# Kernel optimization log

Hardware: AMD Instinct MI355X
Metric: run time of the kernel (lower is better)

Reference implementation:

```python
import jax, jax.numpy as jnp
import numpy as np

B, S, D, H = 2, 2048, 1024, 16
DK = D // H


def setup_inputs() -> dict:
    key = jax.random.key(0)
    ks = jax.random.split(key, 11)
    scale = 1.0 / np.sqrt(D)
    inp = {
        'q': jax.random.normal(ks[0], (B, S, D), jnp.float32),
        'k': jax.random.normal(ks[1], (B, S, D), jnp.float32),
        'v': jax.random.normal(ks[2], (B, S, D), jnp.float32),
        'mask': jnp.tril(jnp.ones((S, S), jnp.int32))[None, None],  # [1,1,S,S] causal
        'w_q': jax.random.normal(ks[3], (D, D), jnp.float32) * scale,
        'b_q': jax.random.normal(ks[4], (D,), jnp.float32) * scale,
        'w_k': jax.random.normal(ks[5], (D, D), jnp.float32) * scale,
        'b_k': jax.random.normal(ks[6], (D,), jnp.float32) * scale,
        'w_v': jax.random.normal(ks[7], (D, D), jnp.float32) * scale,
        'b_v': jax.random.normal(ks[8], (D,), jnp.float32) * scale,
        'w_o': jax.random.normal(ks[9], (D, D), jnp.float32) * scale,
        'b_o': jax.random.normal(ks[10], (D,), jnp.float32) * scale,
    }
    return inp


def reference(q, k, v, mask, w_q, b_q, w_k, b_k, w_v, b_v, w_o, b_o):
    # Linear projections (torch Linear: x @ W^T + b; here weights stored as [D_in, D_out])
    query = q @ w_q + b_q  # [B,S,D]
    key_ = k @ w_k + b_k
    value = v @ w_v + b_v
    # split heads -> [B,H,S,DK]
    def split(x):
        return x.reshape(B, S, H, DK).transpose(0, 2, 1, 3)
    qh, kh, vh = split(query), split(key_), split(value)
    scores = jnp.einsum('bhqd,bhkd->bhqk', qh, kh) / jnp.sqrt(jnp.float32(DK))
    scores = jnp.where(mask == 0, jnp.float32(-1e9), scores)
    attn = jax.nn.softmax(scores, axis=-1)  # dropout p=0.0 -> identity
    out = jnp.einsum('bhqk,bhkd->bhqd', attn, vh)  # [B,H,S,DK]
    out = out.transpose(0, 2, 1, 3).reshape(B, S, D)
    return out @ w_o + b_o
```

## Files before the change

### kernel.cpp

```cpp
#include <hip/hip_runtime.h>

typedef unsigned short u16;
typedef unsigned int u32;
typedef __attribute__((ext_vector_type(8))) short short8;
typedef __attribute__((ext_vector_type(4))) float f32x4;
typedef __attribute__((ext_vector_type(16))) float f32x16;
typedef __attribute__((ext_vector_type(4))) float float4v;
typedef __attribute__((ext_vector_type(4))) u16 u16x4;
typedef __attribute__((ext_vector_type(2))) u32 u32x2;

#define DEV static __device__ __forceinline__

static constexpr int S_LEN = 2048;
static constexpr int D_MODEL = 1024;
static constexpr int N_HEADS = 16;
static constexpr int DK = 64;
static constexpr float LOG2E = 1.4426950408889634f;
static constexpr float SM_SHIFT = 12.0f;

#if defined(__has_builtin)
#if __has_builtin(__builtin_amdgcn_exp2f)
#define EXP2(x) __builtin_amdgcn_exp2f(x)
#else
#define EXP2(x) exp2f(x)
#endif
#else
#define EXP2(x) exp2f(x)
#endif

DEV u16 f2bf(float f) {
  u32 u = __builtin_bit_cast(u32, f);
  u32 r = (u + 0x7FFFu + ((u >> 16) & 1u)) >> 16;
  return (u16)r;
}

DEV u32 pk2bf(float lo, float hi) {
  u32 d;
  asm("v_cvt_pk_bf16_f32 %0, %1, %2" : "=v"(d) : "v"(lo), "v"(hi));
  return d;
}

DEV void swap32(u32& a, u32& b) {
  asm volatile("v_permlane32_swap_b32 %0, %1" : "+v"(a), "+v"(b));
}

DEV short8 mk8(u32 w0, u32 w1, u32 w2, u32 w3) {
  union { u32 u[4]; short8 s; } t;
  t.u[0] = w0; t.u[1] = w1; t.u[2] = w2; t.u[3] = w3;
  return t.s;
}

DEV void async16(const void* g, void* l) {
  __builtin_amdgcn_global_load_lds(
      (const __attribute__((address_space(1))) u32*)g,
      (__attribute__((address_space(3))) u32*)l, 16, 0, 0);
}

DEV short8 lds_frag(const u16* tile, int row, int byteInRow) {
  const char* p = (const char*)tile + row * 128 + (byteInRow ^ ((row & 7) << 4));
  return *(const short8*)p;
}

DEV f32x4 mfma16(short8 a, short8 b, f32x4 c) {
  return __builtin_amdgcn_mfma_f32_16x16x32_bf16(a, b, c, 0, 0, 0);
}

DEV f32x16 mfma32(short8 a, short8 b, f32x16 c) {
  return __builtin_amdgcn_mfma_f32_32x32x16_bf16(a, b, c, 0, 0, 0);
}

__global__ void k_cvt3(const float* __restrict__ q, const float* __restrict__ k,
                       const float* __restrict__ v, u16* __restrict__ xq,
                       u16* __restrict__ xk, u16* __restrict__ xv, int n) {
  const float* src = blockIdx.y == 0 ? q : (blockIdx.y == 1 ? k : v);
  u16* dst = blockIdx.y == 0 ? xq : (blockIdx.y == 1 ? xk : xv);
  int i = (blockIdx.x * blockDim.x + threadIdx.x) * 4;
  int stride = gridDim.x * blockDim.x * 4;
  for (; i < n; i += stride) {
    float4v f = *(const float4v*)(src + i);
    u16x4 o;
    o[0] = f2bf(f[0]); o[1] = f2bf(f[1]); o[2] = f2bf(f[2]); o[3] = f2bf(f[3]);
    *(u16x4*)(dst + i) = o;
  }
}

__global__ void k_twz4(const float* __restrict__ wq, const float* __restrict__ wk,
                       const float* __restrict__ wv, const float* __restrict__ wo,
                       u16* __restrict__ tq, u16* __restrict__ tk,
                       u16* __restrict__ tv, u16* __restrict__ to_) {
  __shared__ u16 t[64][65];
  const int z = blockIdx.z;
  const float* W = z == 0 ? wq : (z == 1 ? wk : (z == 2 ? wv : wo));
  u16* Wt = z == 0 ? tq : (z == 1 ? tk : (z == 2 ? tv : to_));
  const int n0 = blockIdx.x * 64;
  const int k0 = blockIdx.y * 64;
  const int tid = threadIdx.x;
  const int c = tid & 63, r0 = tid >> 6;
#pragma unroll
  for (int j = 0; j < 16; ++j) {
    int r = r0 + j * 4;
    t[r][c] = f2bf(W[(size_t)(k0 + r) * D_MODEL + n0 + c]);
  }
  __syncthreads();
#pragma unroll
  for (int j = 0; j < 16; ++j) {
    int r = r0 + j * 4;
    Wt[(size_t)(n0 + r) * D_MODEL + k0 + c] = t[c][r];
  }
}

__global__ __launch_bounds__(256, 2) void k_gemm3(
    const u16* __restrict__ Xq, const u16* __restrict__ Xk, const u16* __restrict__ Xv,
    const u16* __restrict__ Wtq, const u16* __restrict__ Wtk, const u16* __restrict__ Wtv,
    const float* __restrict__ bq, const float* __restrict__ bk, const float* __restrict__ bv,
    u16* __restrict__ Qh, u16* __restrict__ Kh, u16* __restrict__ Vtp) {
  const int z = blockIdx.z;
  const u16* A = z == 0 ? Xq : (z == 1 ? Xk : Xv);
  const u16* Bt = z == 0 ? Wtq : (z == 1 ? Wtk : Wtv);
  const float* bias = z == 0 ? bq : (z == 1 ? bk : bv);
  u16* obf = z == 0 ? Qh : (z == 1 ? Kh : Vtp);
  const float scale = z == 0 ? 0.125f * LOG2E : 1.0f;

  __shared__ __align__(16) u16 As[128 * 64];
  __shared__ __align__(16) u16 Bs[128 * 64];
  const int tid = threadIdx.x;
  const int lane = tid & 63, w = tid >> 6;
  const int l15 = lane & 15, l4 = lane >> 4;
  const int bm = blockIdx.x * 128, bn = blockIdx.y * 128;
  const int wr = (w >> 1) * 64, wc = (w & 1) * 64;
  const int sr = tid >> 3, sc8 = tid & 7;
  f32x4 acc[4][4] = {};

  for (int k0 = 0; k0 < 1024; k0 += 64) {
    __syncthreads();
#pragma unroll
    for (int j = 0; j < 4; ++j) {
      int row = sr + j * 32;
      int col = (sc8 ^ (row & 7)) << 3;
      async16(A + (size_t)(bm + row) * 1024 + k0 + col, (char*)As + tid * 16 + j * 4096);
      async16(Bt + (size_t)(bn + row) * 1024 + k0 + col, (char*)Bs + tid * 16 + j * 4096);
    }
    __syncthreads();
    short8 af[4][2], bfv[4][2];
#pragma unroll
    for (int mi = 0; mi < 4; ++mi)
#pragma unroll
      for (int kk = 0; kk < 2; ++kk)
        af[mi][kk] = lds_frag(As, wr + mi * 16 + l15, kk * 64 + l4 * 16);
#pragma unroll
    for (int ni = 0; ni < 4; ++ni)
#pragma unroll
      for (int kk = 0; kk < 2; ++kk)
        bfv[ni][kk] = lds_frag(Bs, wc + ni * 16 + l15, kk * 64 + l4 * 16);
#pragma unroll
    for (int kk = 0; kk < 2; ++kk)
#pragma unroll
      for (int mi = 0; mi < 4; ++mi)
#pragma unroll
        for (int ni = 0; ni < 4; ++ni)
          acc[mi][ni] = mfma16(af[mi][kk], bfv[ni][kk], acc[mi][ni]);
  }

#pragma unroll
  for (int mi = 0; mi < 4; ++mi)
#pragma unroll
    for (int ni = 0; ni < 4; ++ni) {
      const int row0 = bm + wr + mi * 16 + l4 * 4;
      const int col = bn + wc + ni * 16 + l15;
      const int h = col >> 6, dk = col & 63;
      const int b = row0 >> 11, s0 = row0 & 2047;
      if (z == 2) {
        u16x4 pk;
#pragma unroll
        for (int r = 0; r < 4; ++r) pk[r] = f2bf(acc[mi][ni][r] + bias[col]);
        *(u16x4*)(obf + ((size_t)((b * N_HEADS + h) * DK + dk)) * S_LEN + s0) = pk;
      } else {
#pragma unroll
        for (int r = 0; r < 4; ++r) {
          float vv = (acc[mi][ni][r] + bias[col]) * scale;
          obf[(((size_t)(b * N_HEADS + h) * S_LEN + s0 + r) << 6) + dk] = f2bf(vv);
        }
      }
    }
}

__global__ __launch_bounds__(256, 2) void k_gemmO(
    const u16* __restrict__ A, const u16* __restrict__ Bt,
    const float* __restrict__ bias, float* __restrict__ ofp) {
  __shared__ __align__(16) u16 As[128 * 64];
  __shared__ __align__(16) u16 Bs[64 * 64];
  const int tid = threadIdx.x;
  const int lane = tid & 63, w = tid >> 6;
  const int l15 = lane & 15, l4 = lane >> 4;
  const int bm = blockIdx.x * 128, bn = blockIdx.y * 64;
  const int wr = w * 32;
  const int sr = tid >> 3, sc8 = tid & 7;
  f32x4 acc[2][4] = {};

  for (int k0 = 0; k0 < 1024; k0 += 64) {
    __syncthreads();
#pragma unroll
    for (int j = 0; j < 4; ++j) {
      int row = sr + j * 32;
      int col = (sc8 ^ (row & 7)) << 3;
      async16(A + (size_t)(bm + row) * 1024 + k0 + col, (char*)As + tid * 16 + j * 4096);
      if (j < 2)
        async16(Bt + (size_t)(bn + row) * 1024 + k0 + col, (char*)Bs + tid * 16 + j * 4096);
    }
    __syncthreads();
    short8 af[2][2], bfv[4][2];
#pragma unroll
    for (int mi = 0; mi < 2; ++mi)
#pragma unroll
      for (int kk = 0; kk < 2; ++kk)
        af[mi][kk] = lds_frag(As, wr + mi * 16 + l15, kk * 64 + l4 * 16);
#pragma unroll
    for (int ni = 0; ni < 4; ++ni)
#pragma unroll
      for (int kk = 0; kk < 2; ++kk)
        bfv[ni][kk] = lds_frag(Bs, ni * 16 + l15, kk * 64 + l4 * 16);
#pragma unroll
    for (int kk = 0; kk < 2; ++kk)
#pragma unroll
      for (int mi = 0; mi < 2; ++mi)
#pragma unroll
        for (int ni = 0; ni < 4; ++ni)
          acc[mi][ni] = mfma16(af[mi][kk], bfv[ni][kk], acc[mi][ni]);
  }

#pragma unroll
  for (int mi = 0; mi < 2; ++mi)
#pragma unroll
    for (int ni = 0; ni < 4; ++ni)
#pragma unroll
      for (int r = 0; r < 4; ++r) {
        int row = bm + wr + mi * 16 + l4 * 4 + r;
        int col = bn + ni * 16 + l15;
        ofp[(size_t)row * D_MODEL + col] = acc[mi][ni][r] + bias[col];
      }
}

__global__ __launch_bounds__(256, 3) void k_attn(
    const u16* __restrict__ Qh, const u16* __restrict__ Kh,
    const u16* __restrict__ Vt, u16* __restrict__ Om,
    float* __restrict__ Po, float* __restrict__ Pl) {
  __shared__ __align__(16) u16 Ks[2][64 * 64];
  __shared__ __align__(16) u16 Vs[2][64 * 64];
  const int tid = threadIdx.x;
  const int lane = tid & 63, w = tid >> 6;
  const int l31 = lane & 31, hf = lane >> 5;
  const int bid = blockIdx.x;

  int bh, g, c, tbeg, tend;
  bool partial;
  if (bid < 256) {
    bh = bid & 31; g = 8 + (bid >> 5); c = 0; tbeg = 0; tend = 16; partial = true;
  } else if (bid < 512) {
    int i = bid - 256;
    bh = i & 31; g = 15 - (i >> 5); c = 1; tbeg = 16; tend = 2 * g + 2; partial = true;
  } else {
    int i = bid - 512;
    bh = i & 31; g = 7 - (i >> 5); c = 0; tbeg = 0; tend = 2 * g + 2; partial = false;
  }

  const u16* Qb = Qh + (size_t)bh * S_LEN * DK;
  const u16* Kb = Kh + (size_t)bh * S_LEN * DK;
  const u16* Vb = Vt + (size_t)bh * DK * S_LEN;
  const int q0 = g * 128;
  const int qw = q0 + w * 32;
  const int sc8 = tid & 7;

  auto stage = [&](int t0, int buf) {
#pragma unroll
    for (int j = 0; j < 2; ++j) {
      int row = (tid >> 3) + j * 32;
      int col = (sc8 ^ (row & 7)) << 3;
      async16(Kb + (size_t)(t0 + row) * DK + col, (char*)Ks[buf] + tid * 16 + j * 4096);
      async16(Vb + (size_t)row * S_LEN + t0 + col, (char*)Vs[buf] + tid * 16 + j * 4096);
    }
  };

  short8 qB[4];
#pragma unroll
  for (int cc = 0; cc < 4; ++cc)
    qB[cc] = *(const short8*)(Qb + (size_t)(qw + l31) * DK + cc * 16 + hf * 8);

  f32x16 od0 = {}, od1 = {};
  float rs = 0.f;

  stage(tbeg << 6, 0);
  __syncthreads();
  int cur = 0;
#pragma unroll 1
  for (int ti = tbeg; ti < tend; ++ti) {
    const int t0 = ti << 6;
    if (ti + 1 < tend) stage((ti + 1) << 6, cur ^ 1);

    f32x16 s0, s1;
#pragma unroll
    for (int r = 0; r < 16; ++r) { s0[r] = -SM_SHIFT; s1[r] = -SM_SHIFT; }
    __builtin_amdgcn_s_setprio(1);
#pragma unroll
    for (int cc = 0; cc < 4; ++cc) {
      short8 k0f = lds_frag(Ks[cur], l31, cc * 32 + hf * 16);
      short8 k1f = lds_frag(Ks[cur], 32 + l31, cc * 32 + hf * 16);
      s0 = mfma32(k0f, qB[cc], s0);
      s1 = mfma32(k1f, qB[cc], s1);
    }
    __builtin_amdgcn_s_setprio(0);

    if (t0 + 63 > qw) {
      const int qrow = qw + l31;
#pragma unroll
      for (int r = 0; r < 16; ++r) {
        int kr = t0 + ((r & 3) + 8 * (r >> 2) + 4 * hf);
        if (kr > qrow) s0[r] = -1e30f;
        if (kr + 32 > qrow) s1[r] = -1e30f;
      }
    }

    float rs0 = 0.f, rs1 = 0.f;
#pragma unroll
    for (int r = 0; r < 16; ++r) {
      s0[r] = EXP2(s0[r]);
      s1[r] = EXP2(s1[r]);
      rs0 += s0[r];
      rs1 += s1[r];
    }
    rs += rs0 + rs1;

    u32 a0 = pk2bf(s0[0], s0[1]), b0 = pk2bf(s0[4], s0[5]);
    u32 c0 = pk2bf(s0[2], s0[3]), d0 = pk2bf(s0[6], s0[7]);
    swap32(a0, b0); swap32(c0, d0);
    short8 pb00 = mk8(a0, c0, b0, d0);
    u32 e0 = pk2bf(s0[8], s0[9]), f0 = pk2bf(s0[12], s0[13]);
    u32 g0 = pk2bf(s0[10], s0[11]), h0 = pk2bf(s0[14], s0[15]);
    swap32(e0, f0); swap32(g0, h0);
    short8 pb01 = mk8(e0, g0, f0, h0);
    u32 a1 = pk2bf(s1[0], s1[1]), b1 = pk2bf(s1[4], s1[5]);
    u32 c1 = pk2bf(s1[2], s1[3]), d1 = pk2bf(s1[6], s1[7]);
    swap32(a1, b1); swap32(c1, d1);
    short8 pb10 = mk8(a1, c1, b1, d1);
    u32 e1 = pk2bf(s1[8], s1[9]), f1 = pk2bf(s1[12], s1[13]);
    u32 g1 = pk2bf(s1[10], s1[11]), h1 = pk2bf(s1[14], s1[15]);
    swap32(e1, f1); swap32(g1, h1);
    short8 pb11 = mk8(e1, g1, f1, h1);

    __builtin_amdgcn_s_setprio(1);
    {
      short8 v00 = lds_frag(Vs[cur], l31, hf * 16);
      short8 v10 = lds_frag(Vs[cur], 32 + l31, hf * 16);
      od0 = mfma32(v00, pb00, od0);
      od1 = mfma32(v10, pb00, od1);
      short8 v01 = lds_frag(Vs[cur], l31, 32 + hf * 16);
      short8 v11 = lds_frag(Vs[cur], 32 + l31, 32 + hf * 16);
      od0 = mfma32(v01, pb01, od0);
      od1 = mfma32(v11, pb01, od1);
      short8 v02 = lds_frag(Vs[cur], l31, 64 + hf * 16);
      short8 v12 = lds_frag(Vs[cur], 32 + l31, 64 + hf * 16);
      od0 = mfma32(v02, pb10, od0);
      od1 = mfma32(v12, pb10, od1);
      short8 v03 = lds_frag(Vs[cur], l31, 96 + hf * 16);
      short8 v13 = lds_frag(Vs[cur], 32 + l31, 96 + hf * 16);
      od0 = mfma32(v03, pb11, od0);
      od1 = mfma32(v13, pb11, od1);
    }
    __builtin_amdgcn_s_setprio(0);
    __syncthreads();
    cur ^= 1;
  }

  rs += __shfl_xor(rs, 32);

  const int qloc = w * 32 + l31;
  if (partial) {
    const int slot = ((bh << 3) + (g - 8)) * 2 + c;
    float* PoS = Po + (size_t)slot * (128 * 64);
#pragma unroll
    for (int rr = 0; rr < 4; ++rr) {
      float4v v0, v1;
#pragma unroll
      for (int i = 0; i < 4; ++i) { v0[i] = od0[rr * 4 + i]; v1[i] = od1[rr * 4 + i]; }
      *(float4v*)(PoS + qloc * 64 + rr * 8 + 4 * hf) = v0;
      *(float4v*)(PoS + qloc * 64 + 32 + rr * 8 + 4 * hf) = v1;
    }
    if (hf == 0) Pl[slot * 128 + qloc] = rs;
  } else {
    const float inv = 1.f / rs;
    const int b = bh >> 4, hd = bh & 15;
    u16* dst = Om + (size_t)(b * S_LEN + qw + l31) * D_MODEL + hd * DK;
#pragma unroll
    for (int rr = 0; rr < 4; ++rr) {
      u16x4 o0, o1;
#pragma unroll
      for (int i = 0; i < 4; ++i) {
        o0[i] = f2bf(od0[rr * 4 + i] * inv);
        o1[i] = f2bf(od1[rr * 4 + i] * inv);
      }
      *(u16x4*)(dst + rr * 8 + 4 * hf) = o0;
      *(u16x4*)(dst + 32 + rr * 8 + 4 * hf) = o1;
    }
  }
}

__global__ void k_comb(const float* __restrict__ Po, const float* __restrict__ Pl,
                       u16* __restrict__ Om) {
  const int bh = blockIdx.x, g8 = blockIdx.y;
  const int tid = threadIdx.x;
  const int slot0 = ((bh << 3) + g8) * 2;
  const float* P0 = Po + (size_t)slot0 * (128 * 64);
  const float* P1 = P0 + (128 * 64);
  const float* L0 = Pl + slot0 * 128;
  const float* L1 = L0 + 128;
  const int b = bh >> 4, h = bh & 15;
  const int row0 = tid >> 4, c4 = (tid & 15) * 4;
#pragma unroll
  for (int j = 0; j < 8; ++j) {
    int row = j * 16 + row0;
    float4v a = *(const float4v*)(P0 + row * 64 + c4);
    float4v bb = *(const float4v*)(P1 + row * 64 + c4);
    float inv = 1.f / (L0[row] + L1[row]);
    u16x4 ov;
#pragma unroll
    for (int i = 0; i < 4; ++i) ov[i] = f2bf((a[i] + bb[i]) * inv);
    int s = 1024 + g8 * 128 + row;
    *(u16x4*)(Om + (size_t)(b * S_LEN + s) * D_MODEL + h * DK + c4) = ov;
  }
}

extern "C" void kernel_launch(void* const* d_in, const int* in_sizes, int n_in,
                              void* d_out, int out_size, void* d_ws, size_t ws_size,
                              hipStream_t stream) {
  (void)in_sizes; (void)n_in; (void)out_size; (void)ws_size;
  const float* q  = (const float*)d_in[0];
  const float* k  = (const float*)d_in[1];
  const float* v  = (const float*)d_in[2];
  const float* wq = (const float*)d_in[4];
  const float* bq = (const float*)d_in[5];
  const float* wk = (const float*)d_in[6];
  const float* bk = (const float*)d_in[7];
  const float* wv = (const float*)d_in[8];
  const float* bv = (const float*)d_in[9];
  const float* wo = (const float*)d_in[10];
  const float* bo = (const float*)d_in[11];
  float* out = (float*)d_out;

  char* ws = (char*)d_ws;
  const size_t XB = (size_t)4096 * 1024 * 2;
  const size_t WB = (size_t)1024 * 1024 * 2;
  u16* Xq  = (u16*)(ws);
  u16* Xk  = (u16*)(ws + XB);
  u16* Xv  = (u16*)(ws + 2 * XB);
  u16* Wtq = (u16*)(ws + 3 * XB);
  u16* Wtk = (u16*)(ws + 3 * XB + WB);
  u16* Wtv = (u16*)(ws + 3 * XB + 2 * WB);
  u16* Wto = (u16*)(ws + 3 * XB + 3 * WB);
  u16* Qh  = (u16*)(ws + 3 * XB + 4 * WB);
  u16* Kh  = (u16*)(ws + 4 * XB + 4 * WB);
  u16* Vtp = (u16*)(ws + 5 * XB + 4 * WB);
  float* Po = (float*)(ws + XB);
  float* Pl = (float*)(ws + 6 * XB + 4 * WB);
  u16* Om  = Xq;

  const int n = 4096 * 1024;
  k_cvt3<<<dim3(512, 3), 256, 0, stream>>>(q, k, v, Xq, Xk, Xv, n);
  k_twz4<<<dim3(16, 16, 4), 256, 0, stream>>>(wq, wk, wv, wo, Wtq, Wtk, Wtv, Wto);
  k_gemm3<<<dim3(32, 8, 3), 256, 0, stream>>>(Xq, Xk, Xv, Wtq, Wtk, Wtv,
                                              bq, bk, bv, Qh, Kh, Vtp);
  k_attn<<<768, 256, 0, stream>>>(Qh, Kh, Vtp, Om, Po, Pl);
  k_comb<<<dim3(32, 8), 256, 0, stream>>>(Po, Pl, Om);
  k_gemmO<<<dim3(32, 16), 256, 0, stream>>>(Om, Wto, bo, out);
}
```

Before: 112.4 us.

## Split causal attention into uniform 8-tile work items with multi-chunk combine

Replaces the old three-way block split (1024-key partial chunks) with a table-driven schedule of 40 items per head, each covering at most 8 key tiles. Query groups needing more than 8 tiles write partials that a generalized combine kernel sums over up to 4 chunks. The inner loop now processes the two 32-key halves one after another to lower register pressure, and launch bounds rise to 4 blocks per SIMD group. The aim is better load balance and occupancy. The cost is more partial-output traffic, a larger combine pass, and a separate workspace region for the partials.

```diff
diff --git a/kernel.cpp b/kernel.cpp
--- a/kernel.cpp
+++ b/kernel.cpp
@@ -7,7 +7,6 @@
 typedef __attribute__((ext_vector_type(16))) float f32x16;
 typedef __attribute__((ext_vector_type(4))) float float4v;
 typedef __attribute__((ext_vector_type(4))) u16 u16x4;
-typedef __attribute__((ext_vector_type(2))) u32 u32x2;
 
 #define DEV static __device__ __forceinline__
 
@@ -240,7 +239,14 @@
       }
 }
 
-__global__ __launch_bounds__(256, 3) void k_attn(
+__device__ __constant__ unsigned char g_item_g[40] = {
+  15,15,15,15, 14,14,14, 13,13,13, 12,12,12, 11,11,11, 10,10, 9,9, 8,8, 7,7,
+  6, 5, 4, 3, 14,10,6,2, 13,9,5,1, 12,8,4,0};
+__device__ __constant__ unsigned char g_item_t0[40] = {
+  0,8,16,24, 0,8,16, 0,8,16, 0,8,16, 0,8,16, 0,8, 0,8, 0,8, 0,8,
+  0, 0, 0, 0, 24,16,8,0, 24,16,8,0, 24,16,8,0};
+
+__global__ __launch_bounds__(256, 4) void k_attn(
     const u16* __restrict__ Qh, const u16* __restrict__ Kh,
     const u16* __restrict__ Vt, u16* __restrict__ Om,
     float* __restrict__ Po, float* __restrict__ Pl) {
@@ -251,17 +257,13 @@
   const int l31 = lane & 31, hf = lane >> 5;
   const int bid = blockIdx.x;
 
-  int bh, g, c, tbeg, tend;
-  bool partial;
-  if (bid < 256) {
-    bh = bid & 31; g = 8 + (bid >> 5); c = 0; tbeg = 0; tend = 16; partial = true;
-  } else if (bid < 512) {
-    int i = bid - 256;
-    bh = i & 31; g = 15 - (i >> 5); c = 1; tbeg = 16; tend = 2 * g + 2; partial = true;
-  } else {
-    int i = bid - 512;
-    bh = i & 31; g = 7 - (i >> 5); c = 0; tbeg = 0; tend = 2 * g + 2; partial = false;
-  }
+  const int bh = bid & 31;
+  const int item = bid >> 5;
+  const int g = g_item_g[item];
+  const int tbeg = g_item_t0[item];
+  const int T = 2 * g + 2;
+  const int tend = min(tbeg + 8, T);
+  const bool partial = T > 8;
 
   const u16* Qb = Qh + (size_t)bh * S_LEN * DK;
   const u16* Kb = Kh + (size_t)bh * S_LEN * DK;
@@ -296,76 +298,60 @@
     const int t0 = ti << 6;
     if (ti + 1 < tend) stage((ti + 1) << 6, cur ^ 1);
 
-    f32x16 s0, s1;
-#pragma unroll
-    for (int r = 0; r < 16; ++r) { s0[r] = -SM_SHIFT; s1[r] = -SM_SHIFT; }
-    __builtin_amdgcn_s_setprio(1);
-#pragma unroll
-    for (int cc = 0; cc < 4; ++cc) {
-      short8 k0f = lds_frag(Ks[cur], l31, cc * 32 + hf * 16);
-      short8 k1f = lds_frag(Ks[cur], 32 + l31, cc * 32 + hf * 16);
-      s0 = mfma32(k0f, qB[cc], s0);
-      s1 = mfma32(k1f, qB[cc], s1);
-    }
-    __builtin_amdgcn_s_setprio(0);
-
-    if (t0 + 63 > qw) {
-      const int qrow = qw + l31;
-#pragma unroll
-      for (int r = 0; r < 16; ++r) {
-        int kr = t0 + ((r & 3) + 8 * (r >> 2) + 4 * hf);
-        if (kr > qrow) s0[r] = -1e30f;
-        if (kr + 32 > qrow) s1[r] = -1e30f;
-      }
-    }
-
-    float rs0 = 0.f, rs1 = 0.f;
-#pragma unroll
-    for (int r = 0; r < 16; ++r) {
-      s0[r] = EXP2(s0[r]);
-      s1[r] = EXP2(s1[r]);
-      rs0 += s0[r];
-      rs1 += s1[r];
-    }
-    rs += rs0 + rs1;
-
-    u32 a0 = pk2bf(s0[0], s0[1]), b0 = pk2bf(s0[4], s0[5]);
-    u32 c0 = pk2bf(s0[2], s0[3]), d0 = pk2bf(s0[6], s0[7]);
-    swap32(a0, b0); swap32(c0, d0);
-    short8 pb00 = mk8(a0, c0, b0, d0);
-    u32 e0 = pk2bf(s0[8], s0[9]), f0 = pk2bf(s0[12], s0[13]);
-    u32 g0 = pk2bf(s0[10], s0[11]), h0 = pk2bf(s0[14], s0[15]);
-    swap32(e0, f0); swap32(g0, h0);
-    short8 pb01 = mk8(e0, g0, f0, h0);
-    u32 a1 = pk2bf(s1[0], s1[1]), b1 = pk2bf(s1[4], s1[5]);
-    u32 c1 = pk2bf(s1[2], s1[3]), d1 = pk2bf(s1[6], s1[7]);
-    swap32(a1, b1); swap32(c1, d1);
-    short8 pb10 = mk8(a1, c1, b1, d1);
-    u32 e1 = pk2bf(s1[8], s1[9]), f1 = pk2bf(s1[12], s1[13]);
-    u32 g1 = pk2bf(s1[10], s1[11]), h1 = pk2bf(s1[14], s1[15]);
-    swap32(e1, f1); swap32(g1, h1);
-    short8 pb11 = mk8(e1, g1, f1, h1);
-
-    __builtin_amdgcn_s_setprio(1);
-    {
-      short8 v00 = lds_frag(Vs[cur], l31, hf * 16);
-      short8 v10 = lds_frag(Vs[cur], 32 + l31, hf * 16);
-      od0 = mfma32(v00, pb00, od0);
-      od1 = mfma32(v10, pb00, od1);
-      short8 v01 = lds_frag(Vs[cur], l31, 32 + hf * 16);
-      short8 v11 = lds_frag(Vs[cur], 32 + l31, 32 + hf * 16);
-      od0 = mfma32(v01, pb01, od0);
-      od1 = mfma32(v11, pb01, od1);
-      short8 v02 = lds_frag(Vs[cur], l31, 64 + hf * 16);
-      short8 v12 = lds_frag(Vs[cur], 32 + l31, 64 + hf * 16);
-      od0 = mfma32(v02, pb10, od0);
-      od1 = mfma32(v12, pb10, od1);
-      short8 v03 = lds_frag(Vs[cur], l31, 96 + hf * 16);
-      short8 v13 = lds_frag(Vs[cur], 32 + l31, 96 + hf * 16);
-      od0 = mfma32(v03, pb11, od0);
-      od1 = mfma32(v13, pb11, od1);
-    }
-    __builtin_amdgcn_s_setprio(0);
+#pragma unroll
+    for (int kt = 0; kt < 2; ++kt) {
+      f32x16 s;
+#pragma unroll
+      for (int r = 0; r < 16; ++r) s[r] = -SM_SHIFT;
+      __builtin_amdgcn_s_setprio(1);
+#pragma unroll
+      for (int cc = 0; cc < 4; ++cc) {
+        short8 kf = lds_frag(Ks[cur], kt * 32 + l31, cc * 32 + hf * 16);
+        s = mfma32(kf, qB[cc], s);
+      }
+      __builtin_amdgcn_s_setprio(0);
+
+      if (t0 + kt * 32 + 31 > qw) {
+        const int qrow = qw + l31;
+#pragma unroll
+        for (int r = 0; r < 16; ++r) {
+          int kr = t0 + kt * 32 + ((r & 3) + 8 * (r >> 2) + 4 * hf);
+          if (kr > qrow) s[r] = -1e30f;
+        }
+      }
+
+#pragma unroll
+      for (int r = 0; r < 16; ++r) s[r] = EXP2(s[r]);
+      {
+        float t01 = (s[0] + s[1]) + (s[2] + s[3]);
+        float t23 = (s[4] + s[5]) + (s[6] + s[7]);
+        float t45 = (s[8] + s[9]) + (s[10] + s[11]);
+        float t67 = (s[12] + s[13]) + (s[14] + s[15]);
+        rs += (t01 + t23) + (t45 + t67);
+      }
+
+      u32 a0 = pk2bf(s[0], s[1]), b0 = pk2bf(s[4], s[5]);
+      u32 c0 = pk2bf(s[2], s[3]), d0 = pk2bf(s[6], s[7]);
+      swap32(a0, b0); swap32(c0, d0);
+      short8 pbA = mk8(a0, c0, b0, d0);
+      u32 e0 = pk2bf(s[8], s[9]), f0 = pk2bf(s[12], s[13]);
+      u32 g0 = pk2bf(s[10], s[11]), h0 = pk2bf(s[14], s[15]);
+      swap32(e0, f0); swap32(g0, h0);
+      short8 pbB = mk8(e0, g0, f0, h0);
+
+      __builtin_amdgcn_s_setprio(1);
+      {
+        short8 v00 = lds_frag(Vs[cur], l31, kt * 64 + hf * 16);
+        short8 v10 = lds_frag(Vs[cur], 32 + l31, kt * 64 + hf * 16);
+        od0 = mfma32(v00, pbA, od0);
+        od1 = mfma32(v10, pbA, od1);
+        short8 v01 = lds_frag(Vs[cur], l31, kt * 64 + 32 + hf * 16);
+        short8 v11 = lds_frag(Vs[cur], 32 + l31, kt * 64 + 32 + hf * 16);
+        od0 = mfma32(v01, pbB, od0);
+        od1 = mfma32(v11, pbB, od1);
+      }
+      __builtin_amdgcn_s_setprio(0);
+    }
     __syncthreads();
     cur ^= 1;
   }
@@ -374,7 +360,7 @@
 
   const int qloc = w * 32 + l31;
   if (partial) {
-    const int slot = ((bh << 3) + (g - 8)) * 2 + c;
+    const int slot = ((bh * 16 + g) << 2) + (tbeg >> 3);
     float* PoS = Po + (size_t)slot * (128 * 64);
 #pragma unroll
     for (int rr = 0; rr < 4; ++rr) {
@@ -405,25 +391,31 @@
 
 __global__ void k_comb(const float* __restrict__ Po, const float* __restrict__ Pl,
                        u16* __restrict__ Om) {
-  const int bh = blockIdx.x, g8 = blockIdx.y;
+  const int bh = blockIdx.x;
+  const int g = 4 + (int)blockIdx.y;
+  const int nch = (2 * g + 2 + 7) >> 3;
   const int tid = threadIdx.x;
-  const int slot0 = ((bh << 3) + g8) * 2;
+  const int slot0 = (bh * 16 + g) << 2;
   const float* P0 = Po + (size_t)slot0 * (128 * 64);
-  const float* P1 = P0 + (128 * 64);
   const float* L0 = Pl + slot0 * 128;
-  const float* L1 = L0 + 128;
   const int b = bh >> 4, h = bh & 15;
   const int row0 = tid >> 4, c4 = (tid & 15) * 4;
 #pragma unroll
   for (int j = 0; j < 8; ++j) {
     int row = j * 16 + row0;
     float4v a = *(const float4v*)(P0 + row * 64 + c4);
-    float4v bb = *(const float4v*)(P1 + row * 64 + c4);
-    float inv = 1.f / (L0[row] + L1[row]);
+    float l = L0[row];
+    for (int c = 1; c < nch; ++c) {
+      float4v bb = *(const float4v*)(P0 + (size_t)c * (128 * 64) + row * 64 + c4);
+#pragma unroll
+      for (int i = 0; i < 4; ++i) a[i] += bb[i];
+      l += L0[c * 128 + row];
+    }
+    float inv = 1.f / l;
     u16x4 ov;
 #pragma unroll
-    for (int i = 0; i < 4; ++i) ov[i] = f2bf((a[i] + bb[i]) * inv);
-    int s = 1024 + g8 * 128 + row;
+    for (int i = 0; i < 4; ++i) ov[i] = f2bf(a[i] * inv);
+    int s = g * 128 + row;
     *(u16x4*)(Om + (size_t)(b * S_LEN + s) * D_MODEL + h * DK + c4) = ov;
   }
 }
@@ -458,8 +450,8 @@
   u16* Qh  = (u16*)(ws + 3 * XB + 4 * WB);
   u16* Kh  = (u16*)(ws + 4 * XB + 4 * WB);
   u16* Vtp = (u16*)(ws + 5 * XB + 4 * WB);
-  float* Po = (float*)(ws + XB);
-  float* Pl = (float*)(ws + 6 * XB + 4 * WB);
+  float* Po = (float*)(ws + 6 * XB + 4 * WB);
+  float* Pl = (float*)(ws + 6 * XB + 4 * WB + (size_t)64 * 1024 * 1024);
   u16* Om  = Xq;
 
   const int n = 4096 * 1024;
@@ -467,7 +459,7 @@
   k_twz4<<<dim3(16, 16, 4), 256, 0, stream>>>(wq, wk, wv, wo, Wtq, Wtk, Wtv, Wto);
   k_gemm3<<<dim3(32, 8, 3), 256, 0, stream>>>(Xq, Xk, Xv, Wtq, Wtk, Wtv,
                                               bq, bk, bv, Qh, Kh, Vtp);
-  k_attn<<<768, 256, 0, stream>>>(Qh, Kh, Vtp, Om, Po, Pl);
-  k_comb<<<dim3(32, 8), 256, 0, stream>>>(Po, Pl, Om);
+  k_attn<<<1280, 256, 0, stream>>>(Qh, Kh, Vtp, Om, Po, Pl);
+  k_comb<<<dim3(32, 12), 256, 0, stream>>>(Po, Pl, Om);
   k_gemmO<<<dim3(32, 16), 256, 0, stream>>>(Om, Wto, bo, out);
 }
```

Measured after the change: 136.2 us. 21.1% more time.
